# Kernel optimization log

Measured on AMD Instinct MI355X. Metric: run time of the kernel, lower is better.

## Reference

```python
import jax, jax.numpy as jnp
import numpy as np

B, S, D = 4, 2048, 1024
H = 16
HD = D // H
PF = 4096
EPS = 1e-5


def setup_inputs() -> dict:
    key = jax.random.key(0)
    ks = jax.random.split(key, 16)
    s = 1.0 / np.sqrt(D)
    inp = {
        'src': jax.random.normal(ks[0], (B, S, D), jnp.float32),
        'Wq': jax.random.normal(ks[1], (D, D), jnp.float32) * s,
        'bq': jnp.zeros((D,), jnp.float32),
        'Wk': jax.random.normal(ks[2], (D, D), jnp.float32) * s,
        'bk': jnp.zeros((D,), jnp.float32),
        'Wv': jax.random.normal(ks[3], (D, D), jnp.float32) * s,
        'bv': jnp.zeros((D,), jnp.float32),
        'Wo': jax.random.normal(ks[4], (D, D), jnp.float32) * s,
        'bo': jnp.zeros((D,), jnp.float32),
        'g1': jnp.ones((D,), jnp.float32),
        'b1': jnp.zeros((D,), jnp.float32),
        'W1': jax.random.normal(ks[5], (D, PF), jnp.float32) * s,
        'bf1': jnp.zeros((PF,), jnp.float32),
        'W2': jax.random.normal(ks[6], (PF, D), jnp.float32) * (1.0 / np.sqrt(PF)),
        'bf2': jnp.zeros((D,), jnp.float32),
        'g2': jnp.ones((D,), jnp.float32),
        'b2': jnp.zeros((D,), jnp.float32),
    }
    return inp


def _layer_norm(x, g, b):
    mu = jnp.mean(x, axis=-1, keepdims=True)
    var = jnp.mean(jnp.square(x - mu), axis=-1, keepdims=True)
    return (x - mu) * jax.lax.rsqrt(var + EPS) * g + b


def reference(src, Wq, bq, Wk, bk, Wv, bv, Wo, bo, g1, b1, W1, bf1, W2, bf2, g2, b2):
    scale = 1.0 / np.sqrt(HD)
    # QKV projections -> [B, H, S, HD]
    q = (src @ Wq + bq).reshape(B, S, H, HD).transpose(0, 2, 1, 3)
    k = (src @ Wk + bk).reshape(B, S, H, HD).transpose(0, 2, 1, 3)
    v = (src @ Wv + bv).reshape(B, S, H, HD).transpose(0, 2, 1, 3)
    # attention scores [B, H, S, S]
    attn = jax.nn.softmax(jnp.einsum('bhqd,bhkd->bhqk', q, k) * scale, axis=-1)
    x = jnp.einsum('bhqk,bhkd->bhqd', attn, v)
    x = x.transpose(0, 2, 1, 3).reshape(B, S, D)
    attn_out = x @ Wo + bo
    # residual + LN (dropout is identity at p=0)
    src1 = _layer_norm(src + attn_out, g1, b1)
    # positionwise FFN: Linear -> Dropout -> ReLU -> Linear
    ff = jax.nn.relu(src1 @ W1 + bf1) @ W2 + bf2
    return _layer_norm(src1 + ff, g2, b2)
```

## Files before the change

kernel.cpp:

```cpp
#include <hip/hip_runtime.h>

#define BB 4
#define SS 2048
#define DD 1024
#define HH 16
#define PFF 4096
#define MR 8192

typedef unsigned short u16;
typedef __attribute__((ext_vector_type(8))) short s16x8;
typedef __attribute__((ext_vector_type(4))) float f32x4v;
typedef __attribute__((ext_vector_type(16))) float f32x16;
typedef __attribute__((ext_vector_type(4))) unsigned short u16x4;
typedef __attribute__((ext_vector_type(8))) unsigned short u16x8;

__device__ inline u16 f2bf(float f) {
  union { float f; unsigned u; } v; v.f = f;
  unsigned r = v.u + 0x7FFFu + ((v.u >> 16) & 1u);
  return (u16)(r >> 16);
}

__device__ inline unsigned cvtpk_bf16(float lo, float hi) {
  unsigned r;
  asm("v_cvt_pk_bf16_f32 %0, %1, %2" : "=v"(r) : "v"(lo), "v"(hi));
  return r;
}

__device__ inline void gload16(const void* g, void* l) {
  __builtin_amdgcn_global_load_lds(
      (const __attribute__((address_space(1))) void*)g,
      (__attribute__((address_space(3))) void*)l, 16, 0, 0);
}

__device__ inline f32x4v MFMA(s16x8 a, s16x8 b, f32x4v c) {
  return __builtin_amdgcn_mfma_f32_16x16x32_bf16(a, b, c, 0, 0, 0);
}
__device__ inline f32x16 MFMA32(s16x8 a, s16x8 b, f32x16 c) {
  return __builtin_amdgcn_mfma_f32_32x32x16_bf16(a, b, c, 0, 0, 0);
}

#define RAWBAR()                          \
  do {                                    \
    asm volatile("" ::: "memory");        \
    __builtin_amdgcn_s_barrier();         \
    asm volatile("" ::: "memory");        \
  } while (0)
#define WAITVM(N) asm volatile("s_waitcnt vmcnt(" #N ")" ::: "memory")

__device__ inline s16x8 ldfrag(const u16* base, int row, int colByte) {
  return *(const s16x8*)((const char*)base + row * 128 + (colByte ^ ((row & 7) << 4)));
}

template <int RELU, int OUTBF>
__global__ __launch_bounds__(512, 1) void gemm256(
    const u16* __restrict__ A, const u16* __restrict__ Bt,
    const float* __restrict__ bias, float* __restrict__ Cf,
    u16* __restrict__ Cb, int M, int N, int K, int ntx) {
  __shared__ __align__(128) u16 lds[3 * 16384];
  const int t = threadIdx.x;
  const int lane = t & 63, w = t >> 6;
  const int wr = w >> 2, wc = w & 3;
  const int g = lane >> 4, q = lane & 15;

  const int cpx = gridDim.x >> 3;
  const int wg = (blockIdx.x & 7) * cpx + (blockIdx.x >> 3);
  const int row0 = (wg / ntx) * 256, col0 = (wg % ntx) * 256;

  f32x4v acc[8][4];
#pragma unroll
  for (int m = 0; m < 8; ++m)
#pragma unroll
    for (int n = 0; n < 4; ++n) acc[m][n] = (f32x4v){0.f, 0.f, 0.f, 0.f};

  const int sr0 = t >> 2, sc0 = (t & 3) * 8;
  const int sr1 = (t + 512) >> 2;
  const u16* Ag0 = A + (size_t)(row0 + sr0) * K + sc0;
  const u16* Ag1 = A + (size_t)(row0 + sr1) * K + sc0;
  const u16* Bg0 = Bt + (size_t)(col0 + sr0) * K + sc0;
  const u16* Bg1 = Bt + (size_t)(col0 + sr1) * K + sc0;
  const int wud = (t & ~63) * 8;

#define STAGE_A(kt, buf)                                          \
  do {                                                            \
    u16* ab_ = &lds[(buf) * 16384];                               \
    gload16(Ag0 + (kt) * 32, ab_ + wud);                          \
    gload16(Ag1 + (kt) * 32, ab_ + 4096 + wud);                   \
  } while (0)
#define STAGE_B(kt, buf)                                          \
  do {                                                            \
    u16* bb_ = &lds[(buf) * 16384 + 8192];                        \
    gload16(Bg0 + (kt) * 32, bb_ + wud);                          \
    gload16(Bg1 + (kt) * 32, bb_ + 4096 + wud);                   \
  } while (0)

  const int NT = K / 32;
  STAGE_A(0, 0); STAGE_B(0, 0);
  STAGE_A(1, 1); STAGE_B(1, 1);
  WAITVM(4);
  RAWBAR();

  int cur = 0, nxt = 2;
  for (int kt = 0; kt < NT; ++kt) {
    const u16* ab = &lds[cur * 16384];
    const u16* bb = ab + 8192;
    const bool pf = (kt + 2 < NT);
    if (pf) STAGE_A(kt + 2, nxt);
    s16x8 bf_[4], af_[4];
#pragma unroll
    for (int n = 0; n < 4; ++n)
      bf_[n] = *(const s16x8*)&bb[(wc * 64 + n * 16 + q) * 32 + g * 8];
#pragma unroll
    for (int m = 0; m < 4; ++m)
      af_[m] = *(const s16x8*)&ab[(wr * 128 + m * 16 + q) * 32 + g * 8];
    RAWBAR();
    __builtin_amdgcn_s_setprio(1);
#pragma unroll
    for (int m = 0; m < 4; ++m)
#pragma unroll
      for (int n = 0; n < 4; ++n) acc[m][n] = MFMA(af_[m], bf_[n], acc[m][n]);
    __builtin_amdgcn_s_setprio(0);
    RAWBAR();
    if (pf) STAGE_B(kt + 2, nxt);
#pragma unroll
    for (int m = 0; m < 4; ++m)
      af_[m] = *(const s16x8*)&ab[(wr * 128 + (m + 4) * 16 + q) * 32 + g * 8];
    RAWBAR();
    __builtin_amdgcn_s_setprio(1);
#pragma unroll
    for (int m = 0; m < 4; ++m)
#pragma unroll
      for (int n = 0; n < 4; ++n) acc[m + 4][n] = MFMA(af_[m], bf_[n], acc[m + 4][n]);
    __builtin_amdgcn_s_setprio(0);
    if (kt + 1 < NT) {
      if (pf) WAITVM(4);
      else WAITVM(0);
    }
    RAWBAR();
    cur = (cur == 2) ? 0 : cur + 1;
    nxt = (nxt == 2) ? 0 : nxt + 1;
  }
#undef STAGE_A
#undef STAGE_B

#pragma unroll
  for (int n = 0; n < 4; ++n) {
    const int col = col0 + wc * 64 + 16 * n + q;
    const float bv = bias[col];
#pragma unroll
    for (int m = 0; m < 8; ++m) {
#pragma unroll
      for (int r = 0; r < 4; ++r) {
        const int row = row0 + wr * 128 + 16 * m + 4 * g + r;
        float v = acc[m][n][r] + bv;
        if (RELU) v = fmaxf(v, 0.f);
        if (OUTBF) Cb[(size_t)row * N + col] = f2bf(v);
        else Cf[(size_t)row * N + col] = v;
      }
    }
  }
}

template <int RELU, int OUTBF>
__global__ __launch_bounds__(256) void gemm_bf16(
    const u16* __restrict__ A, const u16* __restrict__ Bt,
    const float* __restrict__ bias, float* __restrict__ Cf,
    u16* __restrict__ Cb, int M, int N, int K) {
  __shared__ __align__(128) u16 As[128 * 32];
  __shared__ __align__(128) u16 Bs[128 * 32];
  const int t = threadIdx.x;
  const int lane = t & 63, w = t >> 6;
  const int wr = w >> 1, wc = w & 1;
  const int g = lane >> 4, q = lane & 15;
  const int row0 = blockIdx.y * 128, col0 = blockIdx.x * 128;

  f32x4v acc[4][4];
#pragma unroll
  for (int m = 0; m < 4; ++m)
#pragma unroll
    for (int n = 0; n < 4; ++n) acc[m][n] = (f32x4v){0.f, 0.f, 0.f, 0.f};

  const int c0 = t, c1 = 256 + t;
  const int ar0 = c0 >> 2, ac0 = (c0 & 3) * 8;
  const int ar1 = c1 >> 2, ac1 = (c1 & 3) * 8;
  const u16* Ar0 = A + (size_t)(row0 + ar0) * K + ac0;
  const u16* Ar1 = A + (size_t)(row0 + ar1) * K + ac1;
  const u16* Br0 = Bt + (size_t)(col0 + ar0) * K + ac0;
  const u16* Br1 = Bt + (size_t)(col0 + ar1) * K + ac1;
  char* AsB = (char*)As;
  char* BsB = (char*)Bs;
  const int ldst = (t & ~63) * 16;

  for (int k0 = 0; k0 < K; k0 += 32) {
    __syncthreads();
    gload16(Ar0 + k0, AsB + ldst);
    gload16(Ar1 + k0, AsB + 4096 + ldst);
    gload16(Br0 + k0, BsB + ldst);
    gload16(Br1 + k0, BsB + 4096 + ldst);
    __syncthreads();
    s16x8 af[4], bfr[4];
#pragma unroll
    for (int m = 0; m < 4; ++m)
      af[m] = *(const s16x8*)&As[(wr * 64 + 16 * m + q) * 32 + g * 8];
#pragma unroll
    for (int n = 0; n < 4; ++n)
      bfr[n] = *(const s16x8*)&Bs[(wc * 64 + 16 * n + q) * 32 + g * 8];
#pragma unroll
    for (int m = 0; m < 4; ++m)
#pragma unroll
      for (int n = 0; n < 4; ++n) acc[m][n] = MFMA(af[m], bfr[n], acc[m][n]);
  }
#pragma unroll
  for (int n = 0; n < 4; ++n) {
    const int col = col0 + wc * 64 + 16 * n + q;
    const float bv = bias[col];
#pragma unroll
    for (int m = 0; m < 4; ++m) {
#pragma unroll
      for (int r = 0; r < 4; ++r) {
        const int row = row0 + wr * 64 + 16 * m + 4 * g + r;
        float v = acc[m][n][r] + bv;
        if (RELU) v = fmaxf(v, 0.f);
        if (OUTBF) Cb[(size_t)row * N + col] = f2bf(v);
        else Cf[(size_t)row * N + col] = v;
      }
    }
  }
}

__global__ __launch_bounds__(512, 4) void attn_mfma(
    const u16* __restrict__ qkv, const u16* __restrict__ vt,
    u16* __restrict__ xb) {
  __shared__ __align__(128) u16 lds[16384];

  const int t = threadIdx.x;
  const int w = t >> 6, lane = t & 63;
  const int q = lane & 31, hi = lane >> 5;

  const int flat = blockIdx.x;
  const int j = flat >> 3;
  const int bh = (flat & 7) * 8 + (j & 7);
  const int qb = j >> 3;
  const int b = bh >> 4, h = bh & 15;
  const int q0 = qb * 256;
  const int qcol = h * 64, kcol = DD + h * 64;

  const int sr = t >> 3;
  const int sc = ((t & 7) ^ (sr & 7)) * 8;
  const int ldst = (t & ~63) * 16;
  const u16* Ksrc = qkv + (size_t)(b * SS + sr) * 3072 + kcol + sc;
  const u16* Vsrc = vt + (size_t)(bh * 64 + sr) * SS + sc;

  {
    const u16* Qsrc = qkv + (size_t)(b * SS + q0 + sr) * 3072 + qcol + sc;
#pragma unroll
    for (int jj = 0; jj < 4; ++jj)
      gload16(Qsrc + (size_t)jj * 64 * 3072, (char*)lds + jj * 8192 + ldst);
  }
  WAITVM(0);
  RAWBAR();
  s16x8 qf[4];
  {
    const u16* Qw = lds + w * 2048;
#pragma unroll
    for (int s = 0; s < 4; ++s) qf[s] = ldfrag(Qw, q, 32 * s + 16 * hi);
  }
  asm volatile("s_waitcnt lgkmcnt(0)" ::: "memory");
  __builtin_amdgcn_sched_barrier(0);
  RAWBAR();

  gload16(Ksrc, (char*)lds + ldst);
  gload16(Vsrc, (char*)lds + 8192 + ldst);
  WAITVM(0);
  RAWBAR();

  float m_run = -1e30f, l_run = 0.f;
  f32x16 oac0, oac1;
#pragma unroll
  for (int i = 0; i < 16; ++i) { oac0[i] = 0.f; oac1[i] = 0.f; }
  const float SCL2 = 0.18033688011112042f;

  for (int kt = 0; kt < SS / 64; ++kt) {
    const int cur = kt & 1;
    const u16* Kc = lds + cur * 8192;
    const u16* Vc = Kc + 4096;
    if (kt + 1 < SS / 64) {
      const size_t ko = (size_t)(kt + 1) * 64 * 3072;
      const int vo = (kt + 1) * 64;
      gload16(Ksrc + ko, (char*)lds + (cur ^ 1) * 16384 + ldst);
      gload16(Vsrc + vo, (char*)lds + (cur ^ 1) * 16384 + 8192 + ldst);
    }

    f32x16 sa0, sa1;
#pragma unroll
    for (int i = 0; i < 16; ++i) { sa0[i] = 0.f; sa1[i] = 0.f; }
    __builtin_amdgcn_s_setprio(1);
#pragma unroll
    for (int s = 0; s < 4; ++s) {
      s16x8 k0 = ldfrag(Kc, q, 32 * s + 16 * hi);
      s16x8 k1 = ldfrag(Kc, 32 + q, 32 * s + 16 * hi);
      sa0 = MFMA32(k0, qf[s], sa0);
      sa1 = MFMA32(k1, qf[s], sa1);
    }
    __builtin_amdgcn_s_setprio(0);

    float tm = fmaxf(sa0[0], sa1[0]);
#pragma unroll
    for (int i = 1; i < 16; ++i) tm = fmaxf(tm, fmaxf(sa0[i], sa1[i]));
    tm *= SCL2;
    tm = fmaxf(tm, __shfl_xor(tm, 32));
    if (!__all(tm <= m_run + 8.f)) {
      const float m_new = fmaxf(m_run, tm);
      const float rf = exp2f(m_run - m_new);
#pragma unroll
      for (int i = 0; i < 16; ++i) { oac0[i] *= rf; oac1[i] *= rf; }
      l_run *= rf;
      m_run = m_new;
    }
    float psum = 0.f;
#pragma unroll
    for (int i = 0; i < 16; ++i) {
      sa0[i] = exp2f(fmaf(sa0[i], SCL2, -m_run));
      sa1[i] = exp2f(fmaf(sa1[i], SCL2, -m_run));
      psum += sa0[i] + sa1[i];
    }
    psum += __shfl_xor(psum, 32);
    l_run += psum;

    __builtin_amdgcn_s_setprio(1);
#pragma unroll
    for (int s = 0; s < 4; ++s) {
      const int rb = 8 * (s & 1);
      float p0, p1, p2, p3, p4, p5, p6, p7;
      if (s < 2) {
        p0 = sa0[rb]; p1 = sa0[rb + 1]; p2 = sa0[rb + 2]; p3 = sa0[rb + 3];
        p4 = sa0[rb + 4]; p5 = sa0[rb + 5]; p6 = sa0[rb + 6]; p7 = sa0[rb + 7];
      } else {
        p0 = sa1[rb]; p1 = sa1[rb + 1]; p2 = sa1[rb + 2]; p3 = sa1[rb + 3];
        p4 = sa1[rb + 4]; p5 = sa1[rb + 5]; p6 = sa1[rb + 6]; p7 = sa1[rb + 7];
      }
      unsigned a0 = cvtpk_bf16(p0, p1);
      unsigned a1 = cvtpk_bf16(p2, p3);
      unsigned b0 = cvtpk_bf16(p4, p5);
      unsigned b1 = cvtpk_bf16(p6, p7);
      asm("v_permlane32_swap_b32 %0, %1" : "+v"(a0), "+v"(b0));
      asm("v_permlane32_swap_b32 %0, %1" : "+v"(a1), "+v"(b1));
      union { unsigned u[4]; s16x8 v; } pf;
      pf.u[0] = a0; pf.u[1] = a1; pf.u[2] = b0; pf.u[3] = b1;
      s16x8 v0 = ldfrag(Vc, q, 32 * s + 16 * hi);
      s16x8 v1 = ldfrag(Vc, 32 + q, 32 * s + 16 * hi);
      oac0 = MFMA32(v0, pf.v, oac0);
      oac1 = MFMA32(v1, pf.v, oac1);
    }
    __builtin_amdgcn_s_setprio(0);

    WAITVM(0);
    RAWBAR();
  }

  const float inv = 1.f / l_run;
  const size_t row = (size_t)(b * SS + q0 + w * 32 + q);
  u16* orow = xb + row * DD + qcol;
#pragma unroll
  for (int rr = 0; rr < 4; ++rr) {
    uint2 pw0, pw1;
    pw0.x = cvtpk_bf16(oac0[4 * rr] * inv, oac0[4 * rr + 1] * inv);
    pw0.y = cvtpk_bf16(oac0[4 * rr + 2] * inv, oac0[4 * rr + 3] * inv);
    pw1.x = cvtpk_bf16(oac1[4 * rr] * inv, oac1[4 * rr + 1] * inv);
    pw1.y = cvtpk_bf16(oac1[4 * rr + 2] * inv, oac1[4 * rr + 3] * inv);
    *(uint2*)(orow + 8 * rr + 4 * hi) = pw0;
    *(uint2*)(orow + 32 + 8 * rr + 4 * hi) = pw1;
  }
}

__global__ __launch_bounds__(256) void cvt_bf16(const float* __restrict__ x,
                                                u16* __restrict__ y, int n4) {
  int i = blockIdx.x * 256 + threadIdx.x;
  if (i < n4) {
    float4 v = ((const float4*)x)[i];
    u16x4 o;
    o[0] = f2bf(v.x); o[1] = f2bf(v.y); o[2] = f2bf(v.z); o[3] = f2bf(v.w);
    ((u16x4*)y)[i] = o;
  }
}

__global__ __launch_bounds__(256) void transpose_w(const float* __restrict__ W,
                                                   u16* __restrict__ Wt,
                                                   int K, int N) {
  __shared__ float T[32][33];
  const int n0 = blockIdx.x * 32, k0 = blockIdx.y * 32;
  const int t = threadIdx.x;
  const int r = t >> 3, c = (t & 7) * 4;
  float4 v = *(const float4*)&W[(size_t)(k0 + r) * N + n0 + c];
  T[r][c] = v.x; T[r][c + 1] = v.y; T[r][c + 2] = v.z; T[r][c + 3] = v.w;
  __syncthreads();
  const int a = t >> 3, b0 = (t & 7) * 4;
  u16x4 o;
#pragma unroll
  for (int j = 0; j < 4; ++j) o[j] = f2bf(T[b0 + j][a]);
  *(u16x4*)&Wt[(size_t)(n0 + a) * K + k0 + b0] = o;
}

__global__ __launch_bounds__(256) void vtrans(const u16* __restrict__ qkv,
                                              u16* __restrict__ vt) {
  __shared__ u16 T[64 * 72];
  const int t = threadIdx.x;
  const int bh = blockIdx.y, b = bh >> 4, h = bh & 15;
  const int s0 = blockIdx.x * 64;
  const int vcol = 2048 + h * 64;
#pragma unroll
  for (int i = 0; i < 2; ++i) {
    int c = i * 256 + t;
    int sr = c >> 3, dc = (c & 7) * 8;
    *(u16x8*)&T[sr * 72 + dc] =
        *(const u16x8*)&qkv[(size_t)(b * SS + s0 + sr) * 3072 + vcol + dc];
  }
  __syncthreads();
#pragma unroll
  for (int i = 0; i < 2; ++i) {
    int c = i * 256 + t;
    int d = c >> 3, scnk = (c & 7) * 8;
    u16x8 o;
#pragma unroll
    for (int jj = 0; jj < 8; ++jj) o[jj] = T[(scnk + jj) * 72 + d];
    *(u16x8*)&vt[(size_t)(bh * 64 + d) * SS + s0 + scnk] = o;
  }
}

__global__ __launch_bounds__(256) void concat3(const float* __restrict__ a,
                                               const float* __restrict__ b,
                                               const float* __restrict__ c,
                                               float* __restrict__ o) {
  int i = blockIdx.x * 256 + threadIdx.x;
  if (i < 3072)
    o[i] = i < 1024 ? a[i] : (i < 2048 ? b[i - 1024] : c[i - 2048]);
}

template <int WB>
__global__ __launch_bounds__(256) void ln_res(
    const float* __restrict__ X, const float* __restrict__ R,
    const float* __restrict__ g, const float* __restrict__ b,
    float* __restrict__ Y, u16* __restrict__ Yb) {
  const int row = blockIdx.x;
  const int t = threadIdx.x;
  const size_t off = (size_t)row * DD + t * 4;

  float4 x4 = *(const float4*)&X[off];
  float4 r4 = *(const float4*)&R[off];
  float v0 = x4.x + r4.x, v1 = x4.y + r4.y, v2 = x4.z + r4.z, v3 = x4.w + r4.w;

  float s1 = v0 + v1 + v2 + v3;
  float s2 = v0 * v0 + v1 * v1 + v2 * v2 + v3 * v3;
#pragma unroll
  for (int o = 1; o < 64; o <<= 1) {
    s1 += __shfl_xor(s1, o);
    s2 += __shfl_xor(s2, o);
  }
  __shared__ float red1[4], red2[4];
  if ((t & 63) == 0) {
    red1[t >> 6] = s1;
    red2[t >> 6] = s2;
  }
  __syncthreads();
  s1 = red1[0] + red1[1] + red1[2] + red1[3];
  s2 = red2[0] + red2[1] + red2[2] + red2[3];

  const float mu = s1 * (1.f / DD);
  const float var = s2 * (1.f / DD) - mu * mu;
  const float rs = rsqrtf(var + 1e-5f);

  float4 g4 = *(const float4*)&g[t * 4];
  float4 b4 = *(const float4*)&b[t * 4];
  float4 y;
  y.x = (v0 - mu) * rs * g4.x + b4.x;
  y.y = (v1 - mu) * rs * g4.y + b4.y;
  y.z = (v2 - mu) * rs * g4.z + b4.z;
  y.w = (v3 - mu) * rs * g4.w + b4.w;
  *(float4*)&Y[off] = y;
  if (WB) {
    u16x4 o;
    o[0] = f2bf(y.x); o[1] = f2bf(y.y); o[2] = f2bf(y.z); o[3] = f2bf(y.w);
    *(u16x4*)&Yb[off] = o;
  }
}

extern "C" void kernel_launch(void* const* d_in, const int* in_sizes, int n_in,
                              void* d_out, int out_size, void* d_ws,
                              size_t ws_size, hipStream_t stream) {
  const float* src = (const float*)d_in[0];
  const float* Wq  = (const float*)d_in[1];
  const float* bq  = (const float*)d_in[2];
  const float* Wk  = (const float*)d_in[3];
  const float* bk  = (const float*)d_in[4];
  const float* Wv  = (const float*)d_in[5];
  const float* bv  = (const float*)d_in[6];
  const float* Wo  = (const float*)d_in[7];
  const float* bo  = (const float*)d_in[8];
  const float* g1  = (const float*)d_in[9];
  const float* b1  = (const float*)d_in[10];
  const float* W1  = (const float*)d_in[11];
  const float* bf1 = (const float*)d_in[12];
  const float* W2  = (const float*)d_in[13];
  const float* bf2 = (const float*)d_in[14];
  const float* g2  = (const float*)d_in[15];
  const float* b2  = (const float*)d_in[16];

  char* W = (char*)d_ws;
  u16*   wqkvT = (u16*)  (W + 0);
  u16*   woT   = (u16*)  (W + 6291456);
  u16*   w1T   = (u16*)  (W + 8388608);
  u16*   w2T   = (u16*)  (W + 16777216);
  float* bqkv  = (float*)(W + 25165824);
  u16*   srcb  = (u16*)  (W + 25178112);
  u16*   qkv   = (u16*)  (W + 41955328);
  u16*   vt    = (u16*)  (W + 92286976);
  u16*   xb    = (u16*)  (W + 109064192);
  float* pb    = (float*)(W + 125841408);
  float* s1f   = (float*)(W + 159395840);
  u16*   s1bb  = (u16*)  (W + 109064192);
  u16*   f1b   = (u16*)  (W + 41955328);
  float* f2b   = (float*)(W + 125841408);

  dim3 blk(256);

  cvt_bf16<<<8192, blk, 0, stream>>>(src, srcb, MR * DD / 4);
  transpose_w<<<dim3(32, 32), blk, 0, stream>>>(Wq, wqkvT, DD, DD);
  transpose_w<<<dim3(32, 32), blk, 0, stream>>>(Wk, wqkvT + (size_t)1024 * 1024, DD, DD);
  transpose_w<<<dim3(32, 32), blk, 0, stream>>>(Wv, wqkvT + (size_t)2048 * 1024, DD, DD);
  transpose_w<<<dim3(32, 32), blk, 0, stream>>>(Wo, woT, DD, DD);
  transpose_w<<<dim3(128, 32), blk, 0, stream>>>(W1, w1T, DD, PFF);
  transpose_w<<<dim3(32, 128), blk, 0, stream>>>(W2, w2T, PFF, DD);
  concat3<<<12, blk, 0, stream>>>(bq, bk, bv, bqkv);

  gemm256<0, 1><<<384, 512, 0, stream>>>(srcb, wqkvT, bqkv, nullptr, qkv,
                                         MR, 3072, DD, 12);
  vtrans<<<dim3(32, 64), blk, 0, stream>>>(qkv, vt);
  attn_mfma<<<512, 512, 0, stream>>>(qkv, vt, xb);
  gemm_bf16<0, 0><<<dim3(8, 64), blk, 0, stream>>>(xb, woT, bo, pb, nullptr,
                                                   MR, DD, DD);
  ln_res<1><<<MR, blk, 0, stream>>>(src, pb, g1, b1, s1f, s1bb);
  gemm256<1, 1><<<512, 512, 0, stream>>>(s1bb, w1T, bf1, nullptr, f1b,
                                         MR, PFF, DD, 16);
  gemm_bf16<0, 0><<<dim3(8, 64), blk, 0, stream>>>(f1b, w2T, bf2, f2b, nullptr,
                                                   MR, DD, PFF);
  ln_res<0><<<MR, blk, 0, stream>>>(s1f, f2b, g2, b2, (float*)d_out, nullptr);
}
```

Baseline: 488.9 us.

## Use pipelined 256x128 GEMM for N=1024 projections and retile attention blocks

Drops the simple single-buffered 128x128 gemm_bf16 and runs the output projection and second FFN GEMM through a templated version of the triple-buffered 256-row GEMM with 128-wide column tiles. Attention moves to 256-thread blocks handling 128 query rows each, so twice as many blocks are launched. The softmax row sum is now taken with an extra MFMA against a ones vector instead of shuffle reductions, and the row-max reduction is split into parallel chains. The aim is to cut GEMM load stalls and raise attention occupancy, at the cost of one extra MFMA per PV step and smaller grids (256 blocks) for the N=1024 GEMMs.

```diff
diff --git a/kernel.cpp b/kernel.cpp
--- a/kernel.cpp
+++ b/kernel.cpp
@@ -51,89 +51,96 @@
   return *(const s16x8*)((const char*)base + row * 128 + (colByte ^ ((row & 7) << 4)));
 }
 
-template <int RELU, int OUTBF>
+template <int BN, int RELU, int OUTBF>
 __global__ __launch_bounds__(512, 1) void gemm256(
     const u16* __restrict__ A, const u16* __restrict__ Bt,
     const float* __restrict__ bias, float* __restrict__ Cf,
     u16* __restrict__ Cb, int M, int N, int K, int ntx) {
-  __shared__ __align__(128) u16 lds[3 * 16384];
+  constexpr int WM = (BN == 256) ? 8 : 4;
+  constexpr int HM = WM / 2;
+  constexpr int BUF = 8192 + BN * 32;
+  __shared__ __align__(128) u16 lds[3 * BUF];
   const int t = threadIdx.x;
   const int lane = t & 63, w = t >> 6;
-  const int wr = w >> 2, wc = w & 3;
+  const int wr = (BN == 256) ? (w >> 2) : (w >> 1);
+  const int wc = (BN == 256) ? (w & 3) : (w & 1);
   const int g = lane >> 4, q = lane & 15;
 
   const int cpx = gridDim.x >> 3;
   const int wg = (blockIdx.x & 7) * cpx + (blockIdx.x >> 3);
-  const int row0 = (wg / ntx) * 256, col0 = (wg % ntx) * 256;
-
-  f32x4v acc[8][4];
-#pragma unroll
-  for (int m = 0; m < 8; ++m)
+  const int row0 = (wg / ntx) * 256, col0 = (wg % ntx) * BN;
+
+  f32x4v acc[WM][4];
+#pragma unroll
+  for (int m = 0; m < WM; ++m)
 #pragma unroll
     for (int n = 0; n < 4; ++n) acc[m][n] = (f32x4v){0.f, 0.f, 0.f, 0.f};
 
   const int sr0 = t >> 2, sc0 = (t & 3) * 8;
-  const int sr1 = (t + 512) >> 2;
   const u16* Ag0 = A + (size_t)(row0 + sr0) * K + sc0;
-  const u16* Ag1 = A + (size_t)(row0 + sr1) * K + sc0;
+  const u16* Ag1 = A + (size_t)(row0 + sr0 + 128) * K + sc0;
   const u16* Bg0 = Bt + (size_t)(col0 + sr0) * K + sc0;
-  const u16* Bg1 = Bt + (size_t)(col0 + sr1) * K + sc0;
+  const u16* Bg1 = Bt + (size_t)(col0 + sr0 + 128) * K + sc0;
   const int wud = (t & ~63) * 8;
 
 #define STAGE_A(kt, buf)                                          \
   do {                                                            \
-    u16* ab_ = &lds[(buf) * 16384];                               \
+    u16* ab_ = &lds[(buf) * BUF];                                 \
     gload16(Ag0 + (kt) * 32, ab_ + wud);                          \
     gload16(Ag1 + (kt) * 32, ab_ + 4096 + wud);                   \
   } while (0)
 #define STAGE_B(kt, buf)                                          \
   do {                                                            \
-    u16* bb_ = &lds[(buf) * 16384 + 8192];                        \
+    u16* bb_ = &lds[(buf) * BUF + 8192];                          \
     gload16(Bg0 + (kt) * 32, bb_ + wud);                          \
-    gload16(Bg1 + (kt) * 32, bb_ + 4096 + wud);                   \
+    if (BN == 256) gload16(Bg1 + (kt) * 32, bb_ + 4096 + wud);    \
   } while (0)
 
   const int NT = K / 32;
   STAGE_A(0, 0); STAGE_B(0, 0);
   STAGE_A(1, 1); STAGE_B(1, 1);
-  WAITVM(4);
+  if constexpr (BN == 256) WAITVM(4); else WAITVM(3);
   RAWBAR();
 
   int cur = 0, nxt = 2;
   for (int kt = 0; kt < NT; ++kt) {
-    const u16* ab = &lds[cur * 16384];
+    const u16* ab = &lds[cur * BUF];
     const u16* bb = ab + 8192;
     const bool pf = (kt + 2 < NT);
     if (pf) STAGE_A(kt + 2, nxt);
-    s16x8 bf_[4], af_[4];
+    s16x8 bf_[4], af_[HM];
 #pragma unroll
     for (int n = 0; n < 4; ++n)
       bf_[n] = *(const s16x8*)&bb[(wc * 64 + n * 16 + q) * 32 + g * 8];
 #pragma unroll
-    for (int m = 0; m < 4; ++m)
-      af_[m] = *(const s16x8*)&ab[(wr * 128 + m * 16 + q) * 32 + g * 8];
+    for (int m = 0; m < HM; ++m)
+      af_[m] = *(const s16x8*)&ab[(wr * (WM * 16) + m * 16 + q) * 32 + g * 8];
     RAWBAR();
     __builtin_amdgcn_s_setprio(1);
 #pragma unroll
-    for (int m = 0; m < 4; ++m)
+    for (int m = 0; m < HM; ++m)
 #pragma unroll
       for (int n = 0; n < 4; ++n) acc[m][n] = MFMA(af_[m], bf_[n], acc[m][n]);
     __builtin_amdgcn_s_setprio(0);
     RAWBAR();
     if (pf) STAGE_B(kt + 2, nxt);
 #pragma unroll
-    for (int m = 0; m < 4; ++m)
-      af_[m] = *(const s16x8*)&ab[(wr * 128 + (m + 4) * 16 + q) * 32 + g * 8];
+    for (int m = 0; m < HM; ++m)
+      af_[m] = *(const s16x8*)&ab[(wr * (WM * 16) + (m + HM) * 16 + q) * 32 + g * 8];
     RAWBAR();
     __builtin_amdgcn_s_setprio(1);
 #pragma unroll
-    for (int m = 0; m < 4; ++m)
-#pragma unroll
-      for (int n = 0; n < 4; ++n) acc[m + 4][n] = MFMA(af_[m], bf_[n], acc[m + 4][n]);
+    for (int m = 0; m < HM; ++m)
+#pragma unroll
+      for (int n = 0; n < 4; ++n)
+        acc[m + HM][n] = MFMA(af_[m], bf_[n], acc[m + HM][n]);
     __builtin_amdgcn_s_setprio(0);
     if (kt + 1 < NT) {
-      if (pf) WAITVM(4);
-      else WAITVM(0);
+      if (pf) {
+        if constexpr (BN == 256) WAITVM(4); else WAITVM(3);
+      } else {
+        WAITVM(0);
+      }
     }
     RAWBAR();
     cur = (cur == 2) ? 0 : cur + 1;
@@ -147,10 +154,10 @@
     const int col = col0 + wc * 64 + 16 * n + q;
     const float bv = bias[col];
 #pragma unroll
-    for (int m = 0; m < 8; ++m) {
+    for (int m = 0; m < WM; ++m) {
 #pragma unroll
       for (int r = 0; r < 4; ++r) {
-        const int row = row0 + wr * 128 + 16 * m + 4 * g + r;
+        const int row = row0 + wr * (WM * 16) + 16 * m + 4 * g + r;
         float v = acc[m][n][r] + bv;
         if (RELU) v = fmaxf(v, 0.f);
         if (OUTBF) Cb[(size_t)row * N + col] = f2bf(v);
@@ -160,74 +167,7 @@
   }
 }
 
-template <int RELU, int OUTBF>
-__global__ __launch_bounds__(256) void gemm_bf16(
-    const u16* __restrict__ A, const u16* __restrict__ Bt,
-    const float* __restrict__ bias, float* __restrict__ Cf,
-    u16* __restrict__ Cb, int M, int N, int K) {
-  __shared__ __align__(128) u16 As[128 * 32];
-  __shared__ __align__(128) u16 Bs[128 * 32];
-  const int t = threadIdx.x;
-  const int lane = t & 63, w = t >> 6;
-  const int wr = w >> 1, wc = w & 1;
-  const int g = lane >> 4, q = lane & 15;
-  const int row0 = blockIdx.y * 128, col0 = blockIdx.x * 128;
-
-  f32x4v acc[4][4];
-#pragma unroll
-  for (int m = 0; m < 4; ++m)
-#pragma unroll
-    for (int n = 0; n < 4; ++n) acc[m][n] = (f32x4v){0.f, 0.f, 0.f, 0.f};
-
-  const int c0 = t, c1 = 256 + t;
-  const int ar0 = c0 >> 2, ac0 = (c0 & 3) * 8;
-  const int ar1 = c1 >> 2, ac1 = (c1 & 3) * 8;
-  const u16* Ar0 = A + (size_t)(row0 + ar0) * K + ac0;
-  const u16* Ar1 = A + (size_t)(row0 + ar1) * K + ac1;
-  const u16* Br0 = Bt + (size_t)(col0 + ar0) * K + ac0;
-  const u16* Br1 = Bt + (size_t)(col0 + ar1) * K + ac1;
-  char* AsB = (char*)As;
-  char* BsB = (char*)Bs;
-  const int ldst = (t & ~63) * 16;
-
-  for (int k0 = 0; k0 < K; k0 += 32) {
-    __syncthreads();
-    gload16(Ar0 + k0, AsB + ldst);
-    gload16(Ar1 + k0, AsB + 4096 + ldst);
-    gload16(Br0 + k0, BsB + ldst);
-    gload16(Br1 + k0, BsB + 4096 + ldst);
-    __syncthreads();
-    s16x8 af[4], bfr[4];
-#pragma unroll
-    for (int m = 0; m < 4; ++m)
-      af[m] = *(const s16x8*)&As[(wr * 64 + 16 * m + q) * 32 + g * 8];
-#pragma unroll
-    for (int n = 0; n < 4; ++n)
-      bfr[n] = *(const s16x8*)&Bs[(wc * 64 + 16 * n + q) * 32 + g * 8];
-#pragma unroll
-    for (int m = 0; m < 4; ++m)
-#pragma unroll
-      for (int n = 0; n < 4; ++n) acc[m][n] = MFMA(af[m], bfr[n], acc[m][n]);
-  }
-#pragma unroll
-  for (int n = 0; n < 4; ++n) {
-    const int col = col0 + wc * 64 + 16 * n + q;
-    const float bv = bias[col];
-#pragma unroll
-    for (int m = 0; m < 4; ++m) {
-#pragma unroll
-      for (int r = 0; r < 4; ++r) {
-        const int row = row0 + wr * 64 + 16 * m + 4 * g + r;
-        float v = acc[m][n][r] + bv;
-        if (RELU) v = fmaxf(v, 0.f);
-        if (OUTBF) Cb[(size_t)row * N + col] = f2bf(v);
-        else Cf[(size_t)row * N + col] = v;
-      }
-    }
-  }
-}
-
-__global__ __launch_bounds__(512, 4) void attn_mfma(
+__global__ __launch_bounds__(256, 4) void attn_mfma(
     const u16* __restrict__ qkv, const u16* __restrict__ vt,
     u16* __restrict__ xb) {
   __shared__ __align__(128) u16 lds[16384];
@@ -237,24 +177,25 @@
   const int q = lane & 31, hi = lane >> 5;
 
   const int flat = blockIdx.x;
+  const int xcd = flat & 7;
   const int j = flat >> 3;
-  const int bh = (flat & 7) * 8 + (j & 7);
-  const int qb = j >> 3;
+  const int qb = j & 15;
+  const int bh = xcd * 8 + (j >> 4);
   const int b = bh >> 4, h = bh & 15;
-  const int q0 = qb * 256;
+  const int q0 = qb * 128;
   const int qcol = h * 64, kcol = DD + h * 64;
 
-  const int sr = t >> 3;
-  const int sc = ((t & 7) ^ (sr & 7)) * 8;
+  const int r0 = t >> 3;
+  const int sc = ((t & 7) ^ (r0 & 7)) * 8;
   const int ldst = (t & ~63) * 16;
-  const u16* Ksrc = qkv + (size_t)(b * SS + sr) * 3072 + kcol + sc;
-  const u16* Vsrc = vt + (size_t)(bh * 64 + sr) * SS + sc;
+  const u16* Ksrc = qkv + (size_t)(b * SS + r0) * 3072 + kcol + sc;
+  const u16* Vsrc = vt + (size_t)(bh * 64 + r0) * SS + sc;
 
   {
-    const u16* Qsrc = qkv + (size_t)(b * SS + q0 + sr) * 3072 + qcol + sc;
+    const u16* Qsrc = qkv + (size_t)(b * SS + q0 + r0) * 3072 + qcol + sc;
 #pragma unroll
     for (int jj = 0; jj < 4; ++jj)
-      gload16(Qsrc + (size_t)jj * 64 * 3072, (char*)lds + jj * 8192 + ldst);
+      gload16(Qsrc + (size_t)jj * 32 * 3072, (char*)lds + jj * 4096 + ldst);
   }
   WAITVM(0);
   RAWBAR();
@@ -269,14 +210,20 @@
   RAWBAR();
 
   gload16(Ksrc, (char*)lds + ldst);
+  gload16(Ksrc + (size_t)32 * 3072, (char*)lds + 4096 + ldst);
   gload16(Vsrc, (char*)lds + 8192 + ldst);
+  gload16(Vsrc + 32 * SS, (char*)lds + 12288 + ldst);
   WAITVM(0);
   RAWBAR();
 
-  float m_run = -1e30f, l_run = 0.f;
-  f32x16 oac0, oac1;
-#pragma unroll
-  for (int i = 0; i < 16; ++i) { oac0[i] = 0.f; oac1[i] = 0.f; }
+  s16x8 onesv;
+#pragma unroll
+  for (int i = 0; i < 8; ++i) onesv[i] = (short)0x3F80;
+
+  float m_run = -1e30f;
+  f32x16 oac0, oac1, lacc;
+#pragma unroll
+  for (int i = 0; i < 16; ++i) { oac0[i] = 0.f; oac1[i] = 0.f; lacc[i] = 0.f; }
   const float SCL2 = 0.18033688011112042f;
 
   for (int kt = 0; kt < SS / 64; ++kt) {
@@ -286,8 +233,11 @@
     if (kt + 1 < SS / 64) {
       const size_t ko = (size_t)(kt + 1) * 64 * 3072;
       const int vo = (kt + 1) * 64;
-      gload16(Ksrc + ko, (char*)lds + (cur ^ 1) * 16384 + ldst);
-      gload16(Vsrc + vo, (char*)lds + (cur ^ 1) * 16384 + 8192 + ldst);
+      char* base = (char*)lds + (cur ^ 1) * 16384;
+      gload16(Ksrc + ko, base + ldst);
+      gload16(Ksrc + ko + (size_t)32 * 3072, base + 4096 + ldst);
+      gload16(Vsrc + vo, base + 8192 + ldst);
+      gload16(Vsrc + vo + 32 * SS, base + 12288 + ldst);
     }
 
     f32x16 sa0, sa1;
@@ -303,28 +253,36 @@
     }
     __builtin_amdgcn_s_setprio(0);
 
-    float tm = fmaxf(sa0[0], sa1[0]);
-#pragma unroll
-    for (int i = 1; i < 16; ++i) tm = fmaxf(tm, fmaxf(sa0[i], sa1[i]));
-    tm *= SCL2;
+    float pm0 = fmaxf(fmaxf(sa0[0], sa0[1]), sa0[2]);
+    float pm1 = fmaxf(fmaxf(sa0[3], sa0[4]), sa0[5]);
+    float pm2 = fmaxf(fmaxf(sa0[6], sa0[7]), sa0[8]);
+    float pm3 = fmaxf(fmaxf(sa0[9], sa0[10]), sa0[11]);
+    pm0 = fmaxf(fmaxf(pm0, sa0[12]), sa0[13]);
+    pm1 = fmaxf(fmaxf(pm1, sa0[14]), sa0[15]);
+    pm2 = fmaxf(fmaxf(pm2, sa1[0]), sa1[1]);
+    pm3 = fmaxf(fmaxf(pm3, sa1[2]), sa1[3]);
+    pm0 = fmaxf(fmaxf(pm0, sa1[4]), sa1[5]);
+    pm1 = fmaxf(fmaxf(pm1, sa1[6]), sa1[7]);
+    pm2 = fmaxf(fmaxf(pm2, sa1[8]), sa1[9]);
+    pm3 = fmaxf(fmaxf(pm3, sa1[10]), sa1[11]);
+    pm0 = fmaxf(fmaxf(pm0, sa1[12]), sa1[13]);
+    pm1 = fmaxf(fmaxf(pm1, sa1[14]), sa1[15]);
+    float tm = fmaxf(fmaxf(pm0, pm1), fmaxf(pm2, pm3)) * SCL2;
     tm = fmaxf(tm, __shfl_xor(tm, 32));
     if (!__all(tm <= m_run + 8.f)) {
       const float m_new = fmaxf(m_run, tm);
       const float rf = exp2f(m_run - m_new);
 #pragma unroll
-      for (int i = 0; i < 16; ++i) { oac0[i] *= rf; oac1[i] *= rf; }
-      l_run *= rf;
+      for (int i = 0; i < 16; ++i) {
+        oac0[i] *= rf; oac1[i] *= rf; lacc[i] *= rf;
+      }
       m_run = m_new;
     }
-    float psum = 0.f;
 #pragma unroll
     for (int i = 0; i < 16; ++i) {
       sa0[i] = exp2f(fmaf(sa0[i], SCL2, -m_run));
       sa1[i] = exp2f(fmaf(sa1[i], SCL2, -m_run));
-      psum += sa0[i] + sa1[i];
-    }
-    psum += __shfl_xor(psum, 32);
-    l_run += psum;
+    }
 
     __builtin_amdgcn_s_setprio(1);
 #pragma unroll
@@ -350,6 +308,7 @@
       s16x8 v1 = ldfrag(Vc, 32 + q, 32 * s + 16 * hi);
       oac0 = MFMA32(v0, pf.v, oac0);
       oac1 = MFMA32(v1, pf.v, oac1);
+      lacc = MFMA32(onesv, pf.v, lacc);
     }
     __builtin_amdgcn_s_setprio(0);
 
@@ -357,7 +316,7 @@
     RAWBAR();
   }
 
-  const float inv = 1.f / l_run;
+  const float inv = 1.f / lacc[0];
   const size_t row = (size_t)(b * SS + q0 + w * 32 + q);
   u16* orow = xb + row * DD + qcol;
 #pragma unroll
@@ -531,16 +490,16 @@
   transpose_w<<<dim3(32, 128), blk, 0, stream>>>(W2, w2T, PFF, DD);
   concat3<<<12, blk, 0, stream>>>(bq, bk, bv, bqkv);
 
-  gemm256<0, 1><<<384, 512, 0, stream>>>(srcb, wqkvT, bqkv, nullptr, qkv,
-                                         MR, 3072, DD, 12);
+  gemm256<256, 0, 1><<<384, 512, 0, stream>>>(srcb, wqkvT, bqkv, nullptr, qkv,
+                                              MR, 3072, DD, 12);
   vtrans<<<dim3(32, 64), blk, 0, stream>>>(qkv, vt);
-  attn_mfma<<<512, 512, 0, stream>>>(qkv, vt, xb);
-  gemm_bf16<0, 0><<<dim3(8, 64), blk, 0, stream>>>(xb, woT, bo, pb, nullptr,
-                                                   MR, DD, DD);
+  attn_mfma<<<1024, 256, 0, stream>>>(qkv, vt, xb);
+  gemm256<128, 0, 0><<<256, 512, 0, stream>>>(xb, woT, bo, pb, nullptr,
+                                              MR, DD, DD, 8);
   ln_res<1><<<MR, blk, 0, stream>>>(src, pb, g1, b1, s1f, s1bb);
-  gemm256<1, 1><<<512, 512, 0, stream>>>(s1bb, w1T, bf1, nullptr, f1b,
-                                         MR, PFF, DD, 16);
-  gemm_bf16<0, 0><<<dim3(8, 64), blk, 0, stream>>>(f1b, w2T, bf2, f2b, nullptr,
-                                                   MR, DD, PFF);
+  gemm256<256, 1, 1><<<512, 512, 0, stream>>>(s1bb, w1T, bf1, nullptr, f1b,
+                                              MR, PFF, DD, 16);
+  gemm256<128, 0, 0><<<256, 512, 0, stream>>>(f1b, w2T, bf2, f2b, nullptr,
+                                              MR, DD, PFF, 8);
   ln_res<0><<<MR, blk, 0, stream>>>(s1f, f2b, g2, b2, (float*)d_out, nullptr);
 }
```

After: 464.2 us. 1.05x faster.
